# Kernel optimization log

Measured on AMD Instinct MI355X. Metric: run time of the kernel, lower is better.

## Reference

```python
import jax, jax.numpy as jnp
import numpy as np

# Hyperparameters from __init__
TEMPERATURE = 0.07
HARD_POS_W = 1.5
HARD_NEG_W = 2.0
THR_POS = 0.5
THR_NEG = 0.3
NEG_LOSS_W = 0.3

B, D, N_CLASSES = 8192, 256, 1024


def setup_inputs() -> dict:
    key = jax.random.key(0)
    kf, kl = jax.random.split(key)
    features = jax.random.normal(kf, (B, D), dtype=jnp.float32)
    labels = jax.random.randint(kl, (B,), 0, N_CLASSES, dtype=jnp.int32)
    return {"features": features, "labels": labels}


def reference(features, labels):
    b = features.shape[0]
    # L2-normalize features (F.normalize(dim=1))
    anchor = features / jnp.linalg.norm(features, axis=1, keepdims=True)
    sim = anchor @ anchor.T                      # [B, B] cosine similarity
    logits = sim / TEMPERATURE
    logits = logits - jax.lax.stop_gradient(jnp.max(logits, axis=1, keepdims=True))

    mask = (labels[:, None] == labels[None, :]).astype(logits.dtype)   # same-class
    logits_mask = 1.0 - jnp.eye(b, dtype=logits.dtype)                 # exclude self

    # W2ML weights: computed from detached similarities (torch used .item())
    sim_d = jax.lax.stop_gradient(sim)
    offdiag = logits_mask > 0
    is_pos = mask > 0
    hard_pos = is_pos & (sim_d < THR_POS) & offdiag
    pos_weights = jnp.where(
        hard_pos, 1.0 + (THR_POS - sim_d) / THR_POS * (HARD_POS_W - 1.0), 1.0)
    hard_neg = (~is_pos) & (sim_d > THR_NEG) & offdiag
    neg_weights = jnp.where(
        hard_neg, 1.0 + (sim_d - THR_NEG) / (1.0 - THR_NEG) * (HARD_NEG_W - 1.0), 1.0)

    # SupCon log-prob with self excluded from the denominator
    exp_logits = jnp.exp(logits) * logits_mask
    denom = jnp.sum(exp_logits, axis=1, keepdims=True)
    log_prob = logits - jnp.log(denom)

    pos_mask = mask * logits_mask
    pos_cnt = jnp.clip(jnp.sum(pos_mask, axis=1), 1.0, None)
    positive_loss = -jnp.mean(
        jnp.sum(pos_mask * pos_weights * log_prob, axis=1) / pos_cnt)

    # Negative term: weighted mean probability mass assigned to negatives
    neg_mask = (1.0 - mask) * logits_mask
    neg_cnt = jnp.clip(jnp.sum(neg_mask, axis=1), 1.0, None)
    prob = exp_logits / denom
    negative_loss = jnp.mean(
        jnp.sum(neg_mask * neg_weights * prob, axis=1) / neg_cnt)

    return positive_loss + NEG_LOSS_W * negative_loss
```

## Files before the change

kernel.cpp:

```cpp
#include <hip/hip_runtime.h>

#define BSZ  8192
#define DDIM 256
#define BM 128
#define BN 128
#define NT   64
#define NTRI (NT * (NT + 1) / 2)

typedef float f32x4 __attribute__((ext_vector_type(4)));
typedef short bf16x8 __attribute__((ext_vector_type(8)));

__device__ __forceinline__ unsigned short f32_to_bf16(float f) {
    unsigned int u = __float_as_uint(f);
    u += 0x7fffu + ((u >> 16) & 1u);
    return (unsigned short)(u >> 16);
}

#define K_E1   20.60992915555662f
#define K_E2  -20.60992915555662f
#define K_INVT 14.285714285714286f
#define K_N1   1.4285714285714286f
#define K_N2   0.5714285714285714f

__device__ __forceinline__ void decode_tile(int t, int& It, int& Jt) {
    const int off1 = 136, off2 = 392, off3 = 648, off4 = 904, off5 = 1040,
              off6 = 1296, off7 = 1552, off8 = 1688, off9 = 1944;
    int b = (t >= off1) + (t >= off2) + (t >= off3) + (t >= off4) + (t >= off5)
          + (t >= off6) + (t >= off7) + (t >= off8) + (t >= off9);
    int si, sj, r0;
    switch (b) {
        case 0: si = 0; sj = 0; r0 = 0;    break;
        case 1: si = 0; sj = 1; r0 = off1; break;
        case 2: si = 0; sj = 2; r0 = off2; break;
        case 3: si = 0; sj = 3; r0 = off3; break;
        case 4: si = 1; sj = 1; r0 = off4; break;
        case 5: si = 1; sj = 2; r0 = off5; break;
        case 6: si = 1; sj = 3; r0 = off6; break;
        case 7: si = 2; sj = 2; r0 = off7; break;
        case 8: si = 2; sj = 3; r0 = off8; break;
        default: si = 3; sj = 3; r0 = off9; break;
    }
    const int rr = t - r0;
    int il, jl;
    if (si == sj) {
        il = 0;
        #pragma unroll
        for (int q = 1; q < 16; q++) if (rr >= (16 * q - (q * (q - 1)) / 2)) il = q;
        jl = il + (rr - (16 * il - (il * (il - 1)) / 2));
    } else {
        il = rr >> 4;
        jl = rr & 15;
    }
    It = si * 16 + il;
    Jt = sj * 16 + jl;
}

__global__ __launch_bounds__(256) void norm_kernel(const float* __restrict__ feat,
                                                   unsigned short* __restrict__ anchorT,
                                                   float* __restrict__ posAcc,
                                                   unsigned int* __restrict__ counter) {
    __shared__ __align__(16) unsigned short img[32 * 512];
    const int tid  = threadIdx.x;
    const int wid  = tid >> 6;
    const int lane = tid & 63;
    const int R0   = blockIdx.x * 64;

    posAcc[blockIdx.x * 256 + tid] = 0.0f;
    if (blockIdx.x == 0 && tid == 0) *counter = 0u;

    #pragma unroll
    for (int it = 0; it < 16; it++) {
        const int row = R0 + it * 4 + wid;
        const float4 v = ((const float4*)(feat + (size_t)row * DDIM))[lane];
        float ss = v.x * v.x + v.y * v.y + v.z * v.z + v.w * v.w;
        #pragma unroll
        for (int off = 32; off > 0; off >>= 1) ss += __shfl_xor(ss, off, 64);
        const float inv = rsqrtf(ss);
        ushort4 o;
        o.x = f32_to_bf16(v.x * inv);
        o.y = f32_to_bf16(v.y * inv);
        o.z = f32_to_bf16(v.z * inv);
        o.w = f32_to_bf16(v.w * inv);
        const int C    = lane >> 3;
        const int c    = C * 4 + ((row >> 4) & 3);
        const int l16  = (row & 15) + (((lane >> 1) & 3) << 4);
        *(ushort4*)(&img[c * 512 + l16 * 8 + (lane & 1) * 4]) = o;
    }
    __syncthreads();
    #pragma unroll
    for (int p = 0; p < 8; p++) {
        const int c = p * 4 + wid;
        const int T = (c >> 2) * 512 + (R0 >> 4) + (c & 3);
        *(bf16x8*)(anchorT + (size_t)T * 512 + lane * 8) = *(const bf16x8*)(&img[c * 512 + lane * 8]);
    }
}

__device__ __forceinline__ void gload_lds16(const unsigned short* g, unsigned short* l) {
    __builtin_amdgcn_global_load_lds(
        (const __attribute__((address_space(1))) void*)g,
        (__attribute__((address_space(3))) void*)l, 16, 0, 0);
}

__global__ __launch_bounds__(512) void simloss_kernel(
    const unsigned short* __restrict__ anchorT,
    const int* __restrict__ labels,
    float* __restrict__ part,
    float* __restrict__ posAcc)
{
    __shared__ __align__(16) unsigned short As[8 * 512];
    __shared__ __align__(16) unsigned short As2[8 * 512];
    __shared__ __align__(16) unsigned short Bs[8 * 512];
    __shared__ __align__(16) unsigned short Bs2[8 * 512];
    __shared__ float rowDT[2][BM][2];
    __shared__ float colDT[4][BN][2];
    __shared__ int rowLab[BM];
    __shared__ int colLab[BN];

    int It, Jt;
    decode_tile(blockIdx.x, It, Jt);
    const bool diag = (It == Jt);
    const int I0 = It * BM, J0 = Jt * BN;

    const int tid  = threadIdx.x;
    const int lane = tid & 63;
    const int w    = tid >> 6;
    const int rw   = w >> 1;
    const int cw   = w & 1;
    const int cl   = lane & 15;
    const int rg   = lane >> 4;
    const int laneOff = lane * 8;

    if (tid < BM) rowLab[tid] = labels[I0 + tid];
    else if (tid < 2 * BM) colLab[tid - BM] = labels[J0 + tid - BM];

    f32x4 acc[2][4];
    #pragma unroll
    for (int f = 0; f < 2; f++)
        #pragma unroll
        for (int g = 0; g < 4; g++)
            acc[f][g] = (f32x4){0.f, 0.f, 0.f, 0.f};

    #pragma unroll
    for (int kc = 0; kc < 4; kc++) {
        {
            const int C0 = kc * 2;
            const size_t ga0 = ((size_t)C0 * 512 + It * 8) * 512;
            const size_t gb0 = ((size_t)C0 * 512 + Jt * 8) * 512;
            const size_t ga1 = ((size_t)(C0 + 1) * 512 + It * 8) * 512;
            const size_t gb1 = ((size_t)(C0 + 1) * 512 + Jt * 8) * 512;
            gload_lds16(anchorT + ga0 + tid * 8, &As[w * 512]);
            gload_lds16(anchorT + gb0 + tid * 8, &Bs[w * 512]);
            gload_lds16(anchorT + ga1 + tid * 8, &As2[w * 512]);
            gload_lds16(anchorT + gb1 + tid * 8, &Bs2[w * 512]);
        }
        __syncthreads();
        #pragma unroll
        for (int ks = 0; ks < 2; ks++) {
            const unsigned short* aB = (ks == 0 ? As : As2) + (rw * 2) * 512 + laneOff;
            const unsigned short* bB = (ks == 0 ? Bs : Bs2) + (cw * 4) * 512 + laneOff;
            const bf16x8 a0 = *(const bf16x8*)(aB);
            const bf16x8 a1 = *(const bf16x8*)(aB + 512);
            const bf16x8 b0 = *(const bf16x8*)(bB);
            const bf16x8 b1 = *(const bf16x8*)(bB + 512);
            const bf16x8 b2 = *(const bf16x8*)(bB + 1024);
            const bf16x8 b3 = *(const bf16x8*)(bB + 1536);
            acc[0][0] = __builtin_amdgcn_mfma_f32_16x16x32_bf16(a0, b0, acc[0][0], 0, 0, 0);
            acc[0][1] = __builtin_amdgcn_mfma_f32_16x16x32_bf16(a0, b1, acc[0][1], 0, 0, 0);
            acc[0][2] = __builtin_amdgcn_mfma_f32_16x16x32_bf16(a0, b2, acc[0][2], 0, 0, 0);
            acc[0][3] = __builtin_amdgcn_mfma_f32_16x16x32_bf16(a0, b3, acc[0][3], 0, 0, 0);
            acc[1][0] = __builtin_amdgcn_mfma_f32_16x16x32_bf16(a1, b0, acc[1][0], 0, 0, 0);
            acc[1][1] = __builtin_amdgcn_mfma_f32_16x16x32_bf16(a1, b1, acc[1][1], 0, 0, 0);
            acc[1][2] = __builtin_amdgcn_mfma_f32_16x16x32_bf16(a1, b2, acc[1][2], 0, 0, 0);
            acc[1][3] = __builtin_amdgcn_mfma_f32_16x16x32_bf16(a1, b3, acc[1][3], 0, 0, 0);
        }
        __syncthreads();
    }

    int ljr[4], gjr[4];
    #pragma unroll
    for (int g = 0; g < 4; g++) {
        const int cidx = cw * 64 + g * 16 + cl;
        ljr[g] = colLab[cidx];
        gjr[g] = J0 + cidx;
    }
    float cd[4] = {0.f, 0.f, 0.f, 0.f}, ct[4] = {0.f, 0.f, 0.f, 0.f};

    #pragma unroll
    for (int f = 0; f < 2; f++) {
        float rd[4] = {0.f, 0.f, 0.f, 0.f}, rt[4] = {0.f, 0.f, 0.f, 0.f};
        int li[4], gi[4];
        #pragma unroll
        for (int r = 0; r < 4; r++) {
            const int ridx = rw * 32 + f * 16 + rg * 4 + r;
            li[r] = rowLab[ridx];
            gi[r] = I0 + ridx;
        }
        #pragma unroll
        for (int g = 0; g < 4; g++) {
            const int lj = ljr[g];
            const bool granule = (rw * 2 + f) == (cw * 4 + g);
            const f32x4 c = acc[f][g];
            #pragma unroll
            for (int r = 0; r < 4; r++) {
                const float s = c[r];
                const bool self = diag && granule && ((rg * 4 + r) == cl);
                const float e  = self ? 0.f : exp2f(fmaf(s, K_E1, K_E2));
                const float wn = fmaxf(fmaf(s, K_N1, K_N2), 1.0f);
                const float we = wn * e;
                rd[r] += e;  rt[r] += we;
                if (!diag) { cd[g] += e; ct[g] += we; }
                if (li[r] == lj && !self) {
                    const float wp = fmaxf(1.5f - s, 1.0f);
                    const float slp = fmaf(s, K_INVT, -K_INVT) * wp;
                    float* pi = posAcc + (size_t)gi[r] * 4;
                    atomicAdd(pi + 0, slp);
                    atomicAdd(pi + 1, wp);
                    atomicAdd(pi + 2, we);
                    atomicAdd(pi + 3, 1.0f);
                    if (!diag) {
                        float* pj = posAcc + (size_t)gjr[g] * 4;
                        atomicAdd(pj + 0, slp);
                        atomicAdd(pj + 1, wp);
                        atomicAdd(pj + 2, we);
                        atomicAdd(pj + 3, 1.0f);
                    }
                }
            }
        }
        #pragma unroll
        for (int r = 0; r < 4; r++) {
            #pragma unroll
            for (int off = 1; off < 16; off <<= 1) {
                rd[r] += __shfl_xor(rd[r], off, 64);
                rt[r] += __shfl_xor(rt[r], off, 64);
            }
        }
        if (cl == 0) {
            #pragma unroll
            for (int r = 0; r < 4; r++) {
                const int row = rw * 32 + f * 16 + rg * 4 + r;
                rowDT[cw][row][0] = rd[r];
                rowDT[cw][row][1] = rt[r];
            }
        }
    }
    if (!diag) {
        #pragma unroll
        for (int g = 0; g < 4; g++) {
            cd[g] += __shfl_xor(cd[g], 16, 64);
            cd[g] += __shfl_xor(cd[g], 32, 64);
            ct[g] += __shfl_xor(ct[g], 16, 64);
            ct[g] += __shfl_xor(ct[g], 32, 64);
        }
        if (rg == 0) {
            #pragma unroll
            for (int g = 0; g < 4; g++) {
                const int col = cw * 64 + g * 16 + cl;
                colDT[rw][col][0] = cd[g];
                colDT[rw][col][1] = ct[g];
            }
        }
    }

    __syncthreads();
    if (tid < BM) {
        float2 v;
        v.x = rowDT[0][tid][0] + rowDT[1][tid][0];
        v.y = rowDT[0][tid][1] + rowDT[1][tid][1];
        ((float2*)part)[(size_t)Jt * BSZ + I0 + tid] = v;
    } else if (tid < 2 * BM && !diag) {
        const int c = tid - BM;
        float2 v;
        v.x = colDT[0][c][0] + colDT[1][c][0] + colDT[2][c][0] + colDT[3][c][0];
        v.y = colDT[0][c][1] + colDT[1][c][1] + colDT[2][c][1] + colDT[3][c][1];
        ((float2*)part)[(size_t)It * BSZ + J0 + c] = v;
    }
}

__global__ __launch_bounds__(256) void reduce_final_kernel(
    const float* __restrict__ part, const float* __restrict__ posAcc,
    double* __restrict__ partial, unsigned int* __restrict__ counter,
    float* __restrict__ out)
{
    const int i = blockIdx.x * 256 + threadIdx.x;
    float dsum = 0.f, T2 = 0.f;
    const float2* p2 = (const float2*)part;
    #pragma unroll 8
    for (int j = 0; j < NT; j++) {
        const float2 v = p2[(size_t)j * BSZ + i];
        dsum += v.x; T2 += v.y;
    }
    const float4 pa = ((const float4*)posAcc)[i];
    const float s1 = pa.x, w1 = pa.y, s2 = T2 - pa.z, cnt = pa.w;
    const float pc = fmaxf(cnt, 1.0f);
    const float nc = fmaxf(8191.0f - cnt, 1.0f);
    const float ld = logf(dsum);
    const double pos_i = (double)((s1 - ld * w1) / pc);
    const double neg_i = (double)((s2 / dsum) / nc);

    __shared__ double sp[256], sn[256];
    sp[threadIdx.x] = pos_i; sn[threadIdx.x] = neg_i;
    __syncthreads();
    for (int s = 128; s > 0; s >>= 1) {
        if (threadIdx.x < s) {
            sp[threadIdx.x] += sp[threadIdx.x + s];
            sn[threadIdx.x] += sn[threadIdx.x + s];
        }
        __syncthreads();
    }
    __shared__ bool amLast;
    if (threadIdx.x == 0) {
        partial[blockIdx.x * 2 + 0] = sp[0];
        partial[blockIdx.x * 2 + 1] = sn[0];
        __threadfence();
        amLast = (atomicAdd(counter, 1u) == 31u);
    }
    __syncthreads();
    if (amLast) {
        __threadfence();
        const int lane = threadIdx.x;
        double p = 0.0, n = 0.0;
        if (lane < 32) {
            volatile double* vp = (volatile double*)partial;
            p = vp[lane * 2 + 0];
            n = vp[lane * 2 + 1];
        }
        #pragma unroll
        for (int o = 32; o > 0; o >>= 1) { p += __shfl_xor(p, o, 64); n += __shfl_xor(n, o, 64); }
        if (lane == 0) out[0] = (float)(-p / (double)BSZ + 0.3 * (n / (double)BSZ));
    }
}

extern "C" void kernel_launch(void* const* d_in, const int* in_sizes, int n_in,
                              void* d_out, int out_size, void* d_ws, size_t ws_size,
                              hipStream_t stream) {
    const float* feat = (const float*)d_in[0];
    const int* labels = (const int*)d_in[1];
    float* out = (float*)d_out;

    char* ws = (char*)d_ws;
    unsigned short* anchorT = (unsigned short*)ws;
    const size_t anchorBytes = (size_t)BSZ * DDIM * sizeof(unsigned short);
    float* part = (float*)(ws + anchorBytes);
    const size_t partBytes = (size_t)NT * BSZ * 2 * sizeof(float);
    float* posAcc = (float*)(ws + anchorBytes + partBytes);
    const size_t posBytes = (size_t)BSZ * 4 * sizeof(float);
    double* partial = (double*)(ws + anchorBytes + partBytes + posBytes);
    unsigned int* counter = (unsigned int*)(ws + anchorBytes + partBytes + posBytes + 512);

    norm_kernel<<<BSZ / 64, 256, 0, stream>>>(feat, anchorT, posAcc, counter);
    simloss_kernel<<<NTRI, 512, 0, stream>>>(anchorT, labels, part, posAcc);
    reduce_final_kernel<<<BSZ / 256, 256, 0, stream>>>(part, posAcc, partial, counter, out);
}
```

Baseline: 117.3 us.

## Sort rows by label so tiles without positives skip label checks

A single-block counting sort reorders rows by label, and the normalization kernel gathers features in that sorted order. In the similarity kernel, off-diagonal tiles whose label ranges cannot overlap take a branch with no label compares, self checks or atomics. The change also swaps exp2f for a raw v_exp_f32 and spreads the final reduction over more blocks. The cost is an extra serial one-block sort kernel and a gather-style load of feature rows.

Measured after the change: 156.2 us. +33.1%, slower.

```diff
diff --git a/kernel.cpp b/kernel.cpp
--- a/kernel.cpp
+++ b/kernel.cpp
@@ -14,6 +14,12 @@
     unsigned int u = __float_as_uint(f);
     u += 0x7fffu + ((u >> 16) & 1u);
     return (unsigned short)(u >> 16);
+}
+
+__device__ __forceinline__ float fast_exp2(float x) {
+    float r;
+    asm volatile("v_exp_f32 %0, %1" : "=v"(r) : "v"(x));
+    return r;
 }
 
 #define K_E1   20.60992915555662f
@@ -55,23 +61,64 @@
     Jt = sj * 16 + jl;
 }
 
+__global__ __launch_bounds__(256) void sort_kernel(const int* __restrict__ labels,
+                                                   int* __restrict__ s2o,
+                                                   int* __restrict__ sortedLab,
+                                                   unsigned int* __restrict__ counter) {
+    __shared__ int hist[1024];
+    __shared__ int waveSum[4];
+    const int t = threadIdx.x;
+    hist[t] = 0; hist[t + 256] = 0; hist[t + 512] = 0; hist[t + 768] = 0;
+    __syncthreads();
+    for (int i = t; i < BSZ; i += 256) atomicAdd(&hist[labels[i]], 1);
+    __syncthreads();
+    const int h0 = hist[t * 4], h1 = hist[t * 4 + 1], h2 = hist[t * 4 + 2], h3 = hist[t * 4 + 3];
+    const int s = h0 + h1 + h2 + h3;
+    const int lane = t & 63, w = t >> 6;
+    int sc = s;
+    #pragma unroll
+    for (int off = 1; off < 64; off <<= 1) {
+        const int v = __shfl_up(sc, off, 64);
+        if (lane >= off) sc += v;
+    }
+    if (lane == 63) waveSum[w] = sc;
+    __syncthreads();
+    int wbase = 0;
+    #pragma unroll
+    for (int q = 0; q < 4; q++) if (q < w) wbase += waveSum[q];
+    const int excl = wbase + sc - s;
+    hist[t * 4]     = excl;
+    hist[t * 4 + 1] = excl + h0;
+    hist[t * 4 + 2] = excl + h0 + h1;
+    hist[t * 4 + 3] = excl + h0 + h1 + h2;
+    __syncthreads();
+    for (int i = t; i < BSZ; i += 256) {
+        const int c = labels[i];
+        const int p = atomicAdd(&hist[c], 1);
+        s2o[p] = i;
+        sortedLab[p] = c;
+    }
+    if (t == 0) *counter = 0u;
+}
+
 __global__ __launch_bounds__(256) void norm_kernel(const float* __restrict__ feat,
+                                                   const int* __restrict__ s2o,
                                                    unsigned short* __restrict__ anchorT,
-                                                   float* __restrict__ posAcc,
-                                                   unsigned int* __restrict__ counter) {
-    __shared__ __align__(16) unsigned short img[32 * 512];
+                                                   float* __restrict__ posAcc) {
+    __shared__ __align__(16) unsigned short img[8 * 512];
     const int tid  = threadIdx.x;
     const int wid  = tid >> 6;
     const int lane = tid & 63;
-    const int R0   = blockIdx.x * 64;
-
-    posAcc[blockIdx.x * 256 + tid] = 0.0f;
-    if (blockIdx.x == 0 && tid == 0) *counter = 0u;
-
-    #pragma unroll
-    for (int it = 0; it < 16; it++) {
-        const int row = R0 + it * 4 + wid;
-        const float4 v = ((const float4*)(feat + (size_t)row * DDIM))[lane];
+    const int R    = blockIdx.x;
+    const int R0   = R * 16;
+
+    if (tid < 64) posAcc[blockIdx.x * 64 + tid] = 0.0f;
+
+    #pragma unroll
+    for (int it = 0; it < 4; it++) {
+        const int row  = R0 + it * 4 + wid;
+        const int orig = s2o[row];
+        const float4 v = ((const float4*)(feat + (size_t)orig * DDIM))[lane];
         float ss = v.x * v.x + v.y * v.y + v.z * v.z + v.w * v.w;
         #pragma unroll
         for (int off = 32; off > 0; off >>= 1) ss += __shfl_xor(ss, off, 64);
@@ -82,16 +129,15 @@
         o.z = f32_to_bf16(v.z * inv);
         o.w = f32_to_bf16(v.w * inv);
         const int C    = lane >> 3;
-        const int c    = C * 4 + ((row >> 4) & 3);
         const int l16  = (row & 15) + (((lane >> 1) & 3) << 4);
-        *(ushort4*)(&img[c * 512 + l16 * 8 + (lane & 1) * 4]) = o;
-    }
-    __syncthreads();
-    #pragma unroll
-    for (int p = 0; p < 8; p++) {
+        *(ushort4*)(&img[C * 512 + l16 * 8 + (lane & 1) * 4]) = o;
+    }
+    __syncthreads();
+    #pragma unroll
+    for (int p = 0; p < 2; p++) {
         const int c = p * 4 + wid;
-        const int T = (c >> 2) * 512 + (R0 >> 4) + (c & 3);
-        *(bf16x8*)(anchorT + (size_t)T * 512 + lane * 8) = *(const bf16x8*)(&img[c * 512 + lane * 8]);
+        *(bf16x8*)(anchorT + ((size_t)(c * 512 + R)) * 512 + lane * 8) =
+            *(const bf16x8*)(&img[c * 512 + lane * 8]);
     }
 }
 
@@ -103,7 +149,7 @@
 
 __global__ __launch_bounds__(512) void simloss_kernel(
     const unsigned short* __restrict__ anchorT,
-    const int* __restrict__ labels,
+    const int* __restrict__ sortedLab,
     float* __restrict__ part,
     float* __restrict__ posAcc)
 {
@@ -121,6 +167,8 @@
     const bool diag = (It == Jt);
     const int I0 = It * BM, J0 = Jt * BN;
 
+    const bool hasPos = (sortedLab[J0] <= sortedLab[I0 + BM - 1]);
+
     const int tid  = threadIdx.x;
     const int lane = tid & 63;
     const int w    = tid >> 6;
@@ -130,8 +178,10 @@
     const int rg   = lane >> 4;
     const int laneOff = lane * 8;
 
-    if (tid < BM) rowLab[tid] = labels[I0 + tid];
-    else if (tid < 2 * BM) colLab[tid - BM] = labels[J0 + tid - BM];
+    if (hasPos) {
+        if (tid < BM) rowLab[tid] = sortedLab[I0 + tid];
+        else if (tid < 2 * BM) colLab[tid - BM] = sortedLab[J0 + tid - BM];
+    }
 
     f32x4 acc[2][4];
     #pragma unroll
@@ -176,73 +226,102 @@
         __syncthreads();
     }
 
-    int ljr[4], gjr[4];
-    #pragma unroll
-    for (int g = 0; g < 4; g++) {
-        const int cidx = cw * 64 + g * 16 + cl;
-        ljr[g] = colLab[cidx];
-        gjr[g] = J0 + cidx;
-    }
-    float cd[4] = {0.f, 0.f, 0.f, 0.f}, ct[4] = {0.f, 0.f, 0.f, 0.f};
-
-    #pragma unroll
-    for (int f = 0; f < 2; f++) {
-        float rd[4] = {0.f, 0.f, 0.f, 0.f}, rt[4] = {0.f, 0.f, 0.f, 0.f};
-        int li[4], gi[4];
-        #pragma unroll
-        for (int r = 0; r < 4; r++) {
-            const int ridx = rw * 32 + f * 16 + rg * 4 + r;
-            li[r] = rowLab[ridx];
-            gi[r] = I0 + ridx;
-        }
+    float rd[2][4], rt[2][4], cd[4], ct[4];
+    #pragma unroll
+    for (int f = 0; f < 2; f++)
+        #pragma unroll
+        for (int r = 0; r < 4; r++) { rd[f][r] = 0.f; rt[f][r] = 0.f; }
+    #pragma unroll
+    for (int g = 0; g < 4; g++) { cd[g] = 0.f; ct[g] = 0.f; }
+
+    if (!hasPos) {
+        #pragma unroll
+        for (int f = 0; f < 2; f++) {
+            #pragma unroll
+            for (int g = 0; g < 4; g++) {
+                const f32x4 c = acc[f][g];
+                #pragma unroll
+                for (int r = 0; r < 4; r++) {
+                    const float s  = c[r];
+                    const float e  = fast_exp2(fmaf(s, K_E1, K_E2));
+                    const float wn = fmaxf(fmaf(s, K_N1, K_N2), 1.0f);
+                    const float we = wn * e;
+                    rd[f][r] += e;  rt[f][r] += we;
+                    cd[g]    += e;  ct[g]    += we;
+                }
+            }
+        }
+    } else {
+        int ljr[4], gjr[4];
         #pragma unroll
         for (int g = 0; g < 4; g++) {
-            const int lj = ljr[g];
-            const bool granule = (rw * 2 + f) == (cw * 4 + g);
-            const f32x4 c = acc[f][g];
+            const int cidx = cw * 64 + g * 16 + cl;
+            ljr[g] = colLab[cidx];
+            gjr[g] = J0 + cidx;
+        }
+        #pragma unroll
+        for (int f = 0; f < 2; f++) {
+            int li[4], gi[4];
             #pragma unroll
             for (int r = 0; r < 4; r++) {
-                const float s = c[r];
-                const bool self = diag && granule && ((rg * 4 + r) == cl);
-                const float e  = self ? 0.f : exp2f(fmaf(s, K_E1, K_E2));
-                const float wn = fmaxf(fmaf(s, K_N1, K_N2), 1.0f);
-                const float we = wn * e;
-                rd[r] += e;  rt[r] += we;
-                if (!diag) { cd[g] += e; ct[g] += we; }
-                if (li[r] == lj && !self) {
-                    const float wp = fmaxf(1.5f - s, 1.0f);
-                    const float slp = fmaf(s, K_INVT, -K_INVT) * wp;
-                    float* pi = posAcc + (size_t)gi[r] * 4;
-                    atomicAdd(pi + 0, slp);
-                    atomicAdd(pi + 1, wp);
-                    atomicAdd(pi + 2, we);
-                    atomicAdd(pi + 3, 1.0f);
-                    if (!diag) {
-                        float* pj = posAcc + (size_t)gjr[g] * 4;
-                        atomicAdd(pj + 0, slp);
-                        atomicAdd(pj + 1, wp);
-                        atomicAdd(pj + 2, we);
-                        atomicAdd(pj + 3, 1.0f);
+                const int ridx = rw * 32 + f * 16 + rg * 4 + r;
+                li[r] = rowLab[ridx];
+                gi[r] = I0 + ridx;
+            }
+            #pragma unroll
+            for (int g = 0; g < 4; g++) {
+                const int lj = ljr[g];
+                const bool granule = (rw * 2 + f) == (cw * 4 + g);
+                const f32x4 c = acc[f][g];
+                #pragma unroll
+                for (int r = 0; r < 4; r++) {
+                    const float s = c[r];
+                    const bool self = diag && granule && ((rg * 4 + r) == cl);
+                    const float e  = self ? 0.f : fast_exp2(fmaf(s, K_E1, K_E2));
+                    const float wn = fmaxf(fmaf(s, K_N1, K_N2), 1.0f);
+                    const float we = wn * e;
+                    rd[f][r] += e;  rt[f][r] += we;
+                    if (!diag) { cd[g] += e; ct[g] += we; }
+                    if (li[r] == lj && !self) {
+                        const float wp = fmaxf(1.5f - s, 1.0f);
+                        const float slp = fmaf(s, K_INVT, -K_INVT) * wp;
+                        float* pi = posAcc + (size_t)gi[r] * 4;
+                        atomicAdd(pi + 0, slp);
+                        atomicAdd(pi + 1, wp);
+                        atomicAdd(pi + 2, we);
+                        atomicAdd(pi + 3, 1.0f);
+                        if (!diag) {
+                            float* pj = posAcc + (size_t)gjr[g] * 4;
+                            atomicAdd(pj + 0, slp);
+                            atomicAdd(pj + 1, wp);
+                            atomicAdd(pj + 2, we);
+                            atomicAdd(pj + 3, 1.0f);
+                        }
                     }
                 }
             }
         }
+    }
+
+    #pragma unroll
+    for (int f = 0; f < 2; f++)
         #pragma unroll
         for (int r = 0; r < 4; r++) {
             #pragma unroll
             for (int off = 1; off < 16; off <<= 1) {
-                rd[r] += __shfl_xor(rd[r], off, 64);
-                rt[r] += __shfl_xor(rt[r], off, 64);
-            }
-        }
-        if (cl == 0) {
+                rd[f][r] += __shfl_xor(rd[f][r], off, 64);
+                rt[f][r] += __shfl_xor(rt[f][r], off, 64);
+            }
+        }
+    if (cl == 0) {
+        #pragma unroll
+        for (int f = 0; f < 2; f++)
             #pragma unroll
             for (int r = 0; r < 4; r++) {
                 const int row = rw * 32 + f * 16 + rg * 4 + r;
-                rowDT[cw][row][0] = rd[r];
-                rowDT[cw][row][1] = rt[r];
-            }
-        }
+                rowDT[cw][row][0] = rd[f][r];
+                rowDT[cw][row][1] = rt[f][r];
+            }
     }
     if (!diag) {
         #pragma unroll
@@ -282,52 +361,60 @@
     double* __restrict__ partial, unsigned int* __restrict__ counter,
     float* __restrict__ out)
 {
-    const int i = blockIdx.x * 256 + threadIdx.x;
+    const int t   = threadIdx.x;
+    const int row = blockIdx.x * 32 + (t >> 3);
+    const int sg  = t & 7;
     float dsum = 0.f, T2 = 0.f;
     const float2* p2 = (const float2*)part;
-    #pragma unroll 8
-    for (int j = 0; j < NT; j++) {
-        const float2 v = p2[(size_t)j * BSZ + i];
+    #pragma unroll
+    for (int j = 0; j < 8; j++) {
+        const float2 v = p2[(size_t)(sg * 8 + j) * BSZ + row];
         dsum += v.x; T2 += v.y;
     }
-    const float4 pa = ((const float4*)posAcc)[i];
-    const float s1 = pa.x, w1 = pa.y, s2 = T2 - pa.z, cnt = pa.w;
-    const float pc = fmaxf(cnt, 1.0f);
-    const float nc = fmaxf(8191.0f - cnt, 1.0f);
-    const float ld = logf(dsum);
-    const double pos_i = (double)((s1 - ld * w1) / pc);
-    const double neg_i = (double)((s2 / dsum) / nc);
-
-    __shared__ double sp[256], sn[256];
-    sp[threadIdx.x] = pos_i; sn[threadIdx.x] = neg_i;
-    __syncthreads();
-    for (int s = 128; s > 0; s >>= 1) {
-        if (threadIdx.x < s) {
-            sp[threadIdx.x] += sp[threadIdx.x + s];
-            sn[threadIdx.x] += sn[threadIdx.x + s];
-        }
-        __syncthreads();
-    }
+    #pragma unroll
+    for (int off = 1; off < 8; off <<= 1) {
+        dsum += __shfl_xor(dsum, off, 64);
+        T2   += __shfl_xor(T2,   off, 64);
+    }
+    __shared__ double sp[32], sn[32];
+    if (sg == 0) {
+        const float4 pa = ((const float4*)posAcc)[row];
+        const float s1 = pa.x, w1 = pa.y, s2 = T2 - pa.z, cnt = pa.w;
+        const float pc = fmaxf(cnt, 1.0f);
+        const float nc = fmaxf(8191.0f - cnt, 1.0f);
+        const float ld = logf(dsum);
+        sp[t >> 3] = (double)((s1 - ld * w1) / pc);
+        sn[t >> 3] = (double)((s2 / dsum) / nc);
+    }
+    __syncthreads();
     __shared__ bool amLast;
-    if (threadIdx.x == 0) {
-        partial[blockIdx.x * 2 + 0] = sp[0];
-        partial[blockIdx.x * 2 + 1] = sn[0];
-        __threadfence();
-        amLast = (atomicAdd(counter, 1u) == 31u);
+    if (t < 32) {
+        double p = sp[t], n = sn[t];
+        #pragma unroll
+        for (int off = 1; off < 32; off <<= 1) {
+            p += __shfl_xor(p, off, 64);
+            n += __shfl_xor(n, off, 64);
+        }
+        if (t == 0) {
+            partial[blockIdx.x * 2 + 0] = p;
+            partial[blockIdx.x * 2 + 1] = n;
+            __threadfence();
+            amLast = (atomicAdd(counter, 1u) == 255u);
+        }
     }
     __syncthreads();
     if (amLast) {
         __threadfence();
-        const int lane = threadIdx.x;
-        double p = 0.0, n = 0.0;
-        if (lane < 32) {
-            volatile double* vp = (volatile double*)partial;
-            p = vp[lane * 2 + 0];
-            n = vp[lane * 2 + 1];
-        }
-        #pragma unroll
-        for (int o = 32; o > 0; o >>= 1) { p += __shfl_xor(p, o, 64); n += __shfl_xor(n, o, 64); }
-        if (lane == 0) out[0] = (float)(-p / (double)BSZ + 0.3 * (n / (double)BSZ));
+        __shared__ double fp[256], fn[256];
+        volatile double* vp = (volatile double*)partial;
+        fp[t] = vp[t * 2 + 0];
+        fn[t] = vp[t * 2 + 1];
+        __syncthreads();
+        for (int s = 128; s > 0; s >>= 1) {
+            if (t < s) { fp[t] += fp[t + s]; fn[t] += fn[t + s]; }
+            __syncthreads();
+        }
+        if (t == 0) out[0] = (float)(-fp[0] / (double)BSZ + 0.3 * (fn[0] / (double)BSZ));
     }
 }
 
@@ -345,10 +432,14 @@
     const size_t partBytes = (size_t)NT * BSZ * 2 * sizeof(float);
     float* posAcc = (float*)(ws + anchorBytes + partBytes);
     const size_t posBytes = (size_t)BSZ * 4 * sizeof(float);
-    double* partial = (double*)(ws + anchorBytes + partBytes + posBytes);
-    unsigned int* counter = (unsigned int*)(ws + anchorBytes + partBytes + posBytes + 512);
-
-    norm_kernel<<<BSZ / 64, 256, 0, stream>>>(feat, anchorT, posAcc, counter);
-    simloss_kernel<<<NTRI, 512, 0, stream>>>(anchorT, labels, part, posAcc);
-    reduce_final_kernel<<<BSZ / 256, 256, 0, stream>>>(part, posAcc, partial, counter, out);
-}
+    char* p = ws + anchorBytes + partBytes + posBytes;
+    int* s2o       = (int*)p;            p += BSZ * sizeof(int);
+    int* sortedLab = (int*)p;            p += BSZ * sizeof(int);
+    double* partial = (double*)p;        p += 256 * 2 * sizeof(double);
+    unsigned int* counter = (unsigned int*)p;
+
+    sort_kernel<<<1, 256, 0, stream>>>(labels, s2o, sortedLab, counter);
+    norm_kernel<<<BSZ / 16, 256, 0, stream>>>(feat, s2o, anchorT, posAcc);
+    simloss_kernel<<<NTRI, 512, 0, stream>>>(anchorT, sortedLab, part, posAcc);
+    reduce_final_kernel<<<BSZ / 32, 256, 0, stream>>>(part, posAcc, partial, counter, out);
+}
```
